# Kernel optimization log

Measured on AMD Instinct MI355X. Metric: run time of the kernel, lower is better.

## Reference

```python
import jax, jax.numpy as jnp
import numpy as np

B, T, E, H, V, K = 32, 256, 256, 256, 32000, 48
PAD = 0


def setup_inputs() -> dict:
    key = jax.random.key(0)
    ks = jax.random.split(key, 24)
    lengths = jnp.sort(jax.random.randint(ks[0], (B,), 1, T + 1))[::-1]
    lengths = lengths.at[0].set(T)  # pack_padded needs max length present
    sent = jax.random.randint(ks[1], (B, T), 1, V)
    pos = jnp.arange(T)[None, :]
    sentence = jnp.where(pos < lengths[:, None], sent, PAD)
    tags = jax.random.randint(ks[2], (B, T), 0, K)
    s = 0.1
    p = {"sentence": sentence, "lengths": lengths, "tags": tags}
    p["embed"] = jax.random.normal(ks[3], (V, E)) * s
    dims = [E, 2 * H]
    i = 4
    for l in range(2):
        for d in ("f", "b"):
            p[f"Wih_{l}{d}"] = jax.random.normal(ks[i], (4 * H, dims[l])) * s; i += 1
            p[f"Whh_{l}{d}"] = jax.random.normal(ks[i], (4 * H, H)) * s; i += 1
            p[f"b_{l}{d}"] = jax.random.normal(ks[i], (4 * H,)) * s; i += 1
    p["Wout"] = jax.random.normal(ks[i], (K, 2 * H)) * s; i += 1
    p["bout"] = jax.random.normal(ks[i], (K,)) * s; i += 1
    p["start_t"] = jax.random.normal(ks[i], (K,)) * s; i += 1
    p["end_t"] = jax.random.normal(ks[i], (K,)) * s; i += 1
    p["trans"] = jax.random.normal(ks[i], (K, K)) * s
    return p


def _lstm_dir(x, m, Wih, Whh, b, reverse):
    # x: [T,B,D] time-major, m: [T,B] bool. Masked update emulates pack_padded_sequence.
    if reverse:
        x, m = x[::-1], m[::-1]
    Bn, Hn = x.shape[1], Whh.shape[1]

    def step(carry, inp):
        h, c = carry
        xt, mt = inp
        g = xt @ Wih.T + h @ Whh.T + b
        i_, f_, g_, o_ = jnp.split(g, 4, axis=-1)
        c2 = jax.nn.sigmoid(f_) * c + jax.nn.sigmoid(i_) * jnp.tanh(g_)
        h2 = jax.nn.sigmoid(o_) * jnp.tanh(c2)
        mm = mt[:, None]
        h2 = jnp.where(mm, h2, h)
        c2 = jnp.where(mm, c2, c)
        return (h2, c2), jnp.where(mm, h2, 0.0)

    init = (jnp.zeros((Bn, Hn), x.dtype), jnp.zeros((Bn, Hn), x.dtype))
    _, hs = jax.lax.scan(step, init, (x, m))
    return hs[::-1] if reverse else hs


def _forward(sentence, tags, embed, layer_params, Wout, bout, start_t, end_t, trans):
    mask = sentence != PAD                      # [B,T]
    x = embed[sentence]                          # [B,T,E]
    xt = jnp.transpose(x, (1, 0, 2))             # [T,B,E]
    mt = mask.T                                  # [T,B]
    for (Wf, Uf, bf, Wb, Ub, bb) in layer_params:
        hf = _lstm_dir(xt, mt, Wf, Uf, bf, False)
        hb = _lstm_dir(xt, mt, Wb, Ub, bb, True)
        xt = jnp.concatenate([hf, hb], axis=-1)  # [T,B,2H]
    emit = xt @ Wout.T + bout                    # [T,B,K]; dropout is identity in eval

    # ---- CRF log-likelihood (torchcrf) ----
    mf = mt.astype(emit.dtype)
    tt = tags.T                                  # [T,B]
    bar = jnp.arange(sentence.shape[0])
    num = start_t[tt[0]] + emit[0, bar, tt[0]]

    def num_step(s, inp):
        em, tg, pg, m = inp
        return s + (trans[pg, tg] + em[bar, tg]) * m, None

    num, _ = jax.lax.scan(num_step, num, (emit[1:], tt[1:], tt[:-1], mf[1:]))
    last_idx = mf.sum(0).astype(jnp.int32) - 1
    last_tags = tt[last_idx, bar]
    num = num + end_t[last_tags]

    score = start_t[None, :] + emit[0]           # [B,K]

    def den_step(s, inp):
        em, m = inp
        nxt = jax.nn.logsumexp(s[:, :, None] + trans[None] + em[:, None, :], axis=1)
        return jnp.where(m[:, None] > 0, nxt, s), None

    score, _ = jax.lax.scan(den_step, score, (emit[1:], mf[1:]))
    den = jax.nn.logsumexp(score + end_t[None, :], axis=1)
    loss = (num - den).mean()                    # torchcrf reduction='mean' log-likelihood
    return jnp.transpose(emit, (1, 0, 2)), loss, mask


def reference(sentence, lengths, tags, embed,
              Wih_0f, Whh_0f, b_0f, Wih_0b, Whh_0b, b_0b,
              Wih_1f, Whh_1f, b_1f, Wih_1b, Whh_1b, b_1b,
              Wout, bout, start_t, end_t, trans):
    layers = [(Wih_0f, Whh_0f, b_0f, Wih_0b, Whh_0b, b_0b),
              (Wih_1f, Whh_1f, b_1f, Wih_1b, Whh_1b, b_1b)]
    return _forward(sentence, tags, embed, layers, Wout, bout, start_t, end_t, trans)
```

## Files before the change

kernel.cpp:

```cpp
#include <hip/hip_runtime.h>

#define Bz 32
#define Tz 256
#define Ez 256
#define Hz 256
#define Kz 48
#define G4 1024
#define H2 512

typedef __attribute__((ext_vector_type(8))) short short8;
typedef __attribute__((ext_vector_type(4))) float f32x4;
typedef unsigned short ushort_t;
typedef unsigned int uint_t;
typedef unsigned long long ull_t;

__device__ __forceinline__ float bf2f(ushort_t u) {
    unsigned int x = ((unsigned int)u) << 16;
    union { unsigned int i; float f; } c; c.i = x; return c.f;
}
__device__ __forceinline__ ushort_t f2bf(float f) {
    union { float f; unsigned int i; } c; c.f = f;
    unsigned int x = c.i;
    unsigned int lsb = (x >> 16) & 1u;
    x += 0x7fffu + lsb;
    return (ushort_t)(x >> 16);
}
__device__ __forceinline__ float sigm(float x) { return 1.f / (1.f + __expf(-x)); }
__device__ __forceinline__ float tanh_f(float x) { return 1.f - 2.f / (__expf(2.f * x) + 1.f); }

#define MFMA16(a, b, c) __builtin_amdgcn_mfma_f32_16x16x32_bf16((a), (b), (c), 0, 0, 0)

__device__ __forceinline__ void poll8_sweep(const ull_t* b0, const ull_t* b1,
                                            const ull_t* b2, const ull_t* b3,
                                            ull_t* o)
{
    asm volatile(
        "global_load_dwordx2 %0, %8, off sc0 sc1\n\t"
        "global_load_dwordx2 %1, %8, off offset:2048 sc0 sc1\n\t"
        "global_load_dwordx2 %2, %9, off sc0 sc1\n\t"
        "global_load_dwordx2 %3, %9, off offset:2048 sc0 sc1\n\t"
        "global_load_dwordx2 %4, %10, off sc0 sc1\n\t"
        "global_load_dwordx2 %5, %10, off offset:2048 sc0 sc1\n\t"
        "global_load_dwordx2 %6, %11, off sc0 sc1\n\t"
        "global_load_dwordx2 %7, %11, off offset:2048 sc0 sc1\n\t"
        "s_waitcnt vmcnt(0)"
        : "=&v"(o[0]), "=&v"(o[1]), "=&v"(o[2]), "=&v"(o[3]),
          "=&v"(o[4]), "=&v"(o[5]), "=&v"(o[6]), "=&v"(o[7])
        : "v"(b0), "v"(b1), "v"(b2), "v"(b3)
        : "memory");
}

struct CvtArgs {
    const float* s[9];
    ushort_t* d[9];
    int n[9];
};
__global__ __launch_bounds__(256) void cvt_all(CvtArgs a)
{
    int y = blockIdx.y;
    const float* src = a.s[y];
    ushort_t* dst = a.d[y];
    int n = a.n[y];
    int i = (blockIdx.x * 256 + threadIdx.x) * 4;
    if (i < n) {
        float4 v = *(const float4*)(src + i);
        ushort_t o[4] = { f2bf(v.x), f2bf(v.y), f2bf(v.z), f2bf(v.w) };
        *(uint2*)(dst + i) = *(uint2*)o;
    }
}

__global__ __launch_bounds__(64) void embed_kernel(
    const int* __restrict__ sent, const float* __restrict__ embed,
    ushort_t* __restrict__ emb, float* __restrict__ mask_out)
{
    int blk = blockIdx.x;
    int b = blk >> 8, t = blk & 255;
    int s = sent[blk];
    int tid = threadIdx.x;
    float4 v = *(const float4*)(embed + (size_t)s * Ez + tid * 4);
    ushort_t o[4] = { f2bf(v.x), f2bf(v.y), f2bf(v.z), f2bf(v.w) };
    *(uint2*)(emb + ((size_t)t * Bz + b) * Ez + tid * 4) = *(uint2*)o;
    if (tid == 0) mask_out[blk] = (s != 0) ? 1.0f : 0.0f;
}

__global__ __launch_bounds__(256) void gemm_xproj(
    const ushort_t* __restrict__ A,
    const ushort_t* __restrict__ Wf, const ushort_t* __restrict__ Wb,
    const float* __restrict__ biasf, const float* __restrict__ biasb,
    ushort_t* __restrict__ Cf, ushort_t* __restrict__ Cb,
    int M, int Kd)
{
    const ushort_t* W = blockIdx.z ? Wb : Wf;
    const float* bias = blockIdx.z ? biasb : biasf;
    ushort_t* C = blockIdx.z ? Cb : Cf;
    __shared__ __attribute__((aligned(16))) ushort_t sA[128 * 32];
    __shared__ __attribute__((aligned(16))) ushort_t sB[128 * 32];

    int m0 = blockIdx.x * 128, n0 = blockIdx.y * 128;
    int tid = threadIdx.x, l = tid & 63, w = tid >> 6;
    int lr = l & 15, lq = l >> 4;
    int mw = (w & 1) * 64, nw = (w >> 1) * 64;

    int srow_lane = l >> 2;
    int scol_lane = (l & 3) * 8;

    f32x4 acc[4][4] = {};
    for (int ko = 0; ko < Kd; ko += 32) {
        #pragma unroll
        for (int j = 0; j < 4; j++) {
            int seg = w * 4 + j;
            const ushort_t* src;
            ushort_t* dst;
            if (seg < 8) {
                src = A + (size_t)(m0 + seg * 16 + srow_lane) * Kd + ko + scol_lane;
                dst = sA + seg * 512;
            } else {
                src = W + (size_t)(n0 + (seg - 8) * 16 + srow_lane) * Kd + ko + scol_lane;
                dst = sB + (seg - 8) * 512;
            }
            __builtin_amdgcn_global_load_lds(src, dst, 16, 0, 0);
        }
        asm volatile("s_waitcnt vmcnt(0)" ::: "memory");
        __syncthreads();

        short8 af[4], bf_[4];
        #pragma unroll
        for (int mt = 0; mt < 4; mt++)
            af[mt] = *(const short8*)(&sA[(mw + mt * 16 + lr) * 32 + lq * 8]);
        #pragma unroll
        for (int nt = 0; nt < 4; nt++)
            bf_[nt] = *(const short8*)(&sB[(nw + nt * 16 + lr) * 32 + lq * 8]);
        #pragma unroll
        for (int mt = 0; mt < 4; mt++)
            #pragma unroll
            for (int nt = 0; nt < 4; nt++)
                acc[mt][nt] = MFMA16(af[mt], bf_[nt], acc[mt][nt]);
        __syncthreads();
    }

    #pragma unroll
    for (int mt = 0; mt < 4; mt++)
        #pragma unroll
        for (int nt = 0; nt < 4; nt++)
            #pragma unroll
            for (int r = 0; r < 4; r++) {
                int row = m0 + mw + mt * 16 + lq * 4 + r;
                int col = n0 + nw + nt * 16 + lr;
                float v = acc[mt][nt][r] + bias[col];
                C[(size_t)row * G4 + col] = f2bf(v);
            }
}

#define LDK 264

__global__ __launch_bounds__(256, 1) void lstm_layer(
    const ushort_t* __restrict__ Whh_f, const ushort_t* __restrict__ Whh_b,
    const ushort_t* __restrict__ Xp_f, const ushort_t* __restrict__ Xp_b,
    const int* __restrict__ lengths,
    ushort_t* __restrict__ hcat,
    ull_t* __restrict__ hbuf)
{
    __shared__ __attribute__((aligned(16))) ushort_t sH[Bz][LDK];
    __shared__ float sG[4][16][34];

    int bid = blockIdx.x;
    int dir = bid >> 4;
    int sub = bid & 15;
    int h0 = sub * 16;
    const ushort_t* Whh = dir ? Whh_b : Whh_f;
    const ushort_t* Xp  = dir ? Xp_b  : Xp_f;
    int tid = threadIdx.x, l = tid & 63, w = tid >> 6;
    int lr = l & 15, lq = l >> 4;
    int mw = (w & 1) * 16;
    int P  = w >> 1;
    int U0w = h0 + P * 8;

    short8 bw0[8], bw1[8];
    int gA = (lr & 3) * Hz + U0w + (lr >> 2);
    int gB = gA + 4;
    {
        const ushort_t* W0 = Whh + (size_t)gA * Hz;
        const ushort_t* W1 = Whh + (size_t)gB * Hz;
        #pragma unroll
        for (int k = 0; k < 8; k++) {
            bw0[k] = *(const short8*)(W0 + k * 32 + lq * 8);
            bw1[k] = *(const short8*)(W1 + k * 32 + lq * 8);
        }
    }

    int upd = (l < 32);
    int bloc = l & 15;
    int q = (l >> 4) & 1;
    int batch = mw + bloc;
    int lenb = lengths[batch];
    float c4[4] = {0.f, 0.f, 0.f, 0.f};
    ull_t prevw = 0;
    int pubw = batch * 64 + sub * 4 + P * 2 + q;
    int hcoff = dir * Hz + U0w + q * 4;

    for (int s = 0; s < Tz; s++) {
        int t_act = dir ? (Tz - 1 - s) : s;
        const ushort_t* Xrow = Xp + (size_t)t_act * Bz * G4;

        float xv0[4], xv1[4];
        #pragma unroll
        for (int r = 0; r < 4; r++) {
            int brow = mw + lq * 4 + r;
            xv0[r] = bf2f(Xrow[(size_t)brow * G4 + gA]);
            xv1[r] = bf2f(Xrow[(size_t)brow * G4 + gB]);
        }

        const ull_t* hcur = hbuf + ((s & 1) * 2 + dir) * (Bz * Hz / 4);
        const ull_t* b0 = hcur + tid;
        const ull_t* b1 = b0 + 512;
        const ull_t* b2 = b0 + 1024;
        const ull_t* b3 = b0 + 1536;
        uint_t tagc = (uint_t)(((s >> 1) ^ s) & 1);
        ull_t vals[8];
        for (;;) {
            poll8_sweep(b0, b1, b2, b3, vals);
            uint_t ok = 1u;
            #pragma unroll
            for (int k = 0; k < 8; k++)
                ok &= (((uint_t)(vals[k] >> 14) & 1u) == tagc);
            if (ok) break;
        }
        #pragma unroll
        for (int k = 0; k < 8; k++) {
            int idx = k * 256 + tid;
            *(ull_t*)(&sH[idx >> 6][(idx & 63) * 4]) = vals[k] & ~(1ull << 14);
        }
        __syncthreads();

        f32x4 acc0 = {}, acc1 = {};
        #pragma unroll
        for (int k = 0; k < 8; k++) {
            short8 a = *(const short8*)(&sH[mw + lr][k * 32 + lq * 8]);
            acc0 = MFMA16(a, bw0[k], acc0);
            acc1 = MFMA16(a, bw1[k], acc1);
        }
        #pragma unroll
        for (int r = 0; r < 4; r++) {
            sG[w][lq * 4 + r][lr]      = acc0[r] + xv0[r];
            sG[w][lq * 4 + r][16 + lr] = acc1[r] + xv1[r];
        }
        asm volatile("s_waitcnt lgkmcnt(0)" ::: "memory");

        uint_t tagp = (uint_t)((((s + 1) >> 1) ^ (s + 1)) & 1);
        if (upd) {
            int msk = (t_act < lenb);
            ushort_t hx[4], hc[4];
            const ushort_t* ho = (const ushort_t*)&prevw;
            #pragma unroll
            for (int j = 0; j < 4; j++) {
                int cb = q * 16 + j * 4;
                float gi = sG[w][bloc][cb], gf = sG[w][bloc][cb + 1];
                float gg = sG[w][bloc][cb + 2], go = sG[w][bloc][cb + 3];
                float c2 = sigm(gf) * c4[j] + sigm(gi) * tanh_f(gg);
                float h2 = sigm(go) * tanh_f(c2);
                if (msk) c4[j] = c2;
                ushort_t hn = f2bf(h2);
                hx[j] = msk ? hn : ho[j];
                hc[j] = msk ? hn : (ushort_t)0;
            }
            ull_t wd; __builtin_memcpy(&wd, hx, 8);
            prevw = wd;
            wd |= ((ull_t)tagp) << 14;
            ull_t* hnxt = hbuf + (((s + 1) & 1) * 2 + dir) * (Bz * Hz / 4);
            __hip_atomic_store(&hnxt[pubw], wd,
                               __ATOMIC_RELAXED, __HIP_MEMORY_SCOPE_AGENT);
            ull_t wc; __builtin_memcpy(&wc, hc, 8);
            *(ull_t*)(hcat + ((size_t)t_act * Bz + batch) * H2 + hcoff) = wc;
        }
    }
}

__global__ __launch_bounds__(256) void gemm_emit(
    const ushort_t* __restrict__ A, const ushort_t* __restrict__ Wout,
    const float* __restrict__ bout, float* __restrict__ emit_out)
{
    int tid = threadIdx.x, l = tid & 63, w = tid >> 6;
    int m0 = blockIdx.x * 64 + w * 16;
    int lr = l & 15, lq = l >> 4;
    f32x4 acc[3] = {};
    for (int ko = 0; ko < H2; ko += 32) {
        short8 a = *(const short8*)(A + (size_t)(m0 + lr) * H2 + ko + lq * 8);
        #pragma unroll
        for (int nt = 0; nt < 3; nt++) {
            short8 bfr = *(const short8*)(Wout + (size_t)(nt * 16 + lr) * H2 + ko + lq * 8);
            acc[nt] = MFMA16(a, bfr, acc[nt]);
        }
    }
    #pragma unroll
    for (int nt = 0; nt < 3; nt++)
        #pragma unroll
        for (int r = 0; r < 4; r++) {
            int row = m0 + lq * 4 + r;
            int col = nt * 16 + lr;
            float v = acc[nt][r] + bout[col];
            int t = row >> 5, b = row & 31;
            emit_out[((size_t)b * Tz + t) * Kz + col] = v;
        }
}

__global__ __launch_bounds__(256) void crf_num(
    const float* __restrict__ emit, const int* __restrict__ sent,
    const int* __restrict__ tags, const int* __restrict__ lengths,
    const float* __restrict__ trans, const float* __restrict__ start_t,
    const float* __restrict__ end_t, float* __restrict__ num)
{
    __shared__ float red[4];
    int b = blockIdx.x, t = threadIdx.x;
    int tg = tags[b * Tz + t];
    float term;
    if (t == 0) {
        term = start_t[tg] + emit[(size_t)b * Tz * Kz + tg];
        int len = lengths[b];
        term += end_t[tags[b * Tz + len - 1]];
    } else if (sent[b * Tz + t] != 0) {
        int tp = tags[b * Tz + t - 1];
        term = trans[tp * Kz + tg] + emit[((size_t)b * Tz + t) * Kz + tg];
    } else term = 0.f;
    #pragma unroll
    for (int off = 1; off < 64; off <<= 1) term += __shfl_xor(term, off);
    int w = t >> 6;
    if ((t & 63) == 0) red[w] = term;
    __syncthreads();
    if (t == 0) num[b] = red[0] + red[1] + red[2] + red[3];
}

__global__ __launch_bounds__(64) void crf_den(
    const float* __restrict__ emit, const int* __restrict__ lengths,
    const float* __restrict__ trans, const float* __restrict__ start_t,
    const float* __restrict__ end_t, float* __restrict__ den)
{
    __shared__ float sT[Kz * Kz];
    __shared__ float sS[Kz];
    int b = blockIdx.x, l = threadIdx.x;
    for (int i = l; i < Kz * Kz; i += 64) sT[i] = trans[i];
    int len = lengths[b];
    bool act = l < Kz;
    float s = act ? (start_t[l] + emit[(size_t)b * Tz * Kz + l]) : -1e30f;
    for (int t = 1; t < len; t++) {
        float em = act ? emit[((size_t)b * Tz + t) * Kz + l] : 0.f;
        if (act) sS[l] = s;
        float M = s;
        #pragma unroll
        for (int off = 1; off < 64; off <<= 1) M = fmaxf(M, __shfl_xor(M, off));
        float a0 = 0.f, a1 = 0.f, a2 = 0.f, a3 = 0.f;
        #pragma unroll 4
        for (int i = 0; i < Kz; i += 4) {
            a0 += __expf(sS[i]     + sT[i * Kz + l]       - M);
            a1 += __expf(sS[i + 1] + sT[(i + 1) * Kz + l] - M);
            a2 += __expf(sS[i + 2] + sT[(i + 2) * Kz + l] - M);
            a3 += __expf(sS[i + 3] + sT[(i + 3) * Kz + l] - M);
        }
        float sum = (a0 + a1) + (a2 + a3);
        if (act) s = em + M + __logf(sum);
    }
    float v = act ? (s + end_t[l]) : -1e30f;
    float M = v;
    #pragma unroll
    for (int off = 1; off < 64; off <<= 1) M = fmaxf(M, __shfl_xor(M, off));
    float accv = act ? __expf(v - M) : 0.f;
    #pragma unroll
    for (int off = 1; off < 64; off <<= 1) accv += __shfl_xor(accv, off);
    if (l == 0) den[b] = M + __logf(accv);
}

__global__ __launch_bounds__(64) void crf_loss(
    const float* __restrict__ num, const float* __restrict__ den, float* __restrict__ out)
{
    int l = threadIdx.x;
    float v = (l < Bz) ? (num[l] - den[l]) : 0.f;
    #pragma unroll
    for (int off = 1; off < 64; off <<= 1) v += __shfl_xor(v, off);
    if (l == 0) out[0] = v / (float)Bz;
}

extern "C" void kernel_launch(void* const* d_in, const int* in_sizes, int n_in,
                              void* d_out, int out_size, void* d_ws, size_t ws_size,
                              hipStream_t stream) {
    const int* sent      = (const int*)d_in[0];
    const int* lengths   = (const int*)d_in[1];
    const int* tags      = (const int*)d_in[2];
    const float* embed   = (const float*)d_in[3];
    const float* Wih0f = (const float*)d_in[4];
    const float* Whh0f = (const float*)d_in[5];
    const float* b0f   = (const float*)d_in[6];
    const float* Wih0b = (const float*)d_in[7];
    const float* Whh0b = (const float*)d_in[8];
    const float* b0b   = (const float*)d_in[9];
    const float* Wih1f = (const float*)d_in[10];
    const float* Whh1f = (const float*)d_in[11];
    const float* b1f   = (const float*)d_in[12];
    const float* Wih1b = (const float*)d_in[13];
    const float* Whh1b = (const float*)d_in[14];
    const float* b1b   = (const float*)d_in[15];
    const float* Wout  = (const float*)d_in[16];
    const float* bout  = (const float*)d_in[17];
    const float* start_t = (const float*)d_in[18];
    const float* end_t   = (const float*)d_in[19];
    const float* trans   = (const float*)d_in[20];

    char* ws = (char*)d_ws;
    ushort_t* Xp_f  = (ushort_t*)(ws);
    ushort_t* Xp_b  = (ushort_t*)(ws + 16777216);
    ushort_t* hcat  = (ushort_t*)(ws + 33554432);
    ushort_t* emb   = (ushort_t*)(ws + 41943040);
    ushort_t* Whh0f_c = (ushort_t*)(ws + 46137344);
    ushort_t* Whh0b_c = (ushort_t*)(ws + 46661632);
    ushort_t* Wih0f_c = (ushort_t*)(ws + 47185920);
    ushort_t* Wih0b_c = (ushort_t*)(ws + 47710208);
    ushort_t* Wih1f_c = (ushort_t*)(ws + 48234496);
    ushort_t* Wih1b_c = (ushort_t*)(ws + 49283072);
    ushort_t* Whh1f_c = (ushort_t*)(ws + 50331648);
    ushort_t* Whh1b_c = (ushort_t*)(ws + 50855936);
    ushort_t* Wout_c  = (ushort_t*)(ws + 51380224);
    ull_t*    hbufL0 = (ull_t*)(ws + 51429376);
    ull_t*    hbufL1 = (ull_t*)(ws + 51560448);
    float*    num   = (float*)   (ws + 51691520);
    float*    den   = (float*)   (ws + 51691776);

    float* out      = (float*)d_out;
    float* loss_out = out + (size_t)Bz * Tz * Kz;
    float* mask_out = loss_out + 1;

    hipMemsetAsync(hbufL0, 0, 262144, stream);

    CvtArgs ca;
    ca.s[0] = Whh0f; ca.d[0] = Whh0f_c; ca.n[0] = 262144;
    ca.s[1] = Whh0b; ca.d[1] = Whh0b_c; ca.n[1] = 262144;
    ca.s[2] = Wih0f; ca.d[2] = Wih0f_c; ca.n[2] = 262144;
    ca.s[3] = Wih0b; ca.d[3] = Wih0b_c; ca.n[3] = 262144;
    ca.s[4] = Wih1f; ca.d[4] = Wih1f_c; ca.n[4] = 524288;
    ca.s[5] = Wih1b; ca.d[5] = Wih1b_c; ca.n[5] = 524288;
    ca.s[6] = Whh1f; ca.d[6] = Whh1f_c; ca.n[6] = 262144;
    ca.s[7] = Whh1b; ca.d[7] = Whh1b_c; ca.n[7] = 262144;
    ca.s[8] = Wout;  ca.d[8] = Wout_c;  ca.n[8] = 24576;
    cvt_all<<<dim3(512, 9), 256, 0, stream>>>(ca);

    embed_kernel<<<Bz * Tz, 64, 0, stream>>>(sent, embed, emb, mask_out);

    gemm_xproj<<<dim3(Tz * Bz / 128, G4 / 128, 2), 256, 0, stream>>>(
        emb, Wih0f_c, Wih0b_c, b0f, b0b, Xp_f, Xp_b, Tz * Bz, Ez);

    lstm_layer<<<32, 256, 0, stream>>>(Whh0f_c, Whh0b_c, Xp_f, Xp_b, lengths, hcat, hbufL0);

    gemm_xproj<<<dim3(Tz * Bz / 128, G4 / 128, 2), 256, 0, stream>>>(
        hcat, Wih1f_c, Wih1b_c, b1f, b1b, Xp_f, Xp_b, Tz * Bz, H2);

    lstm_layer<<<32, 256, 0, stream>>>(Whh1f_c, Whh1b_c, Xp_f, Xp_b, lengths, hcat, hbufL1);

    gemm_emit<<<Tz * Bz / 64, 256, 0, stream>>>(hcat, Wout_c, bout, out);

    crf_num<<<Bz, 256, 0, stream>>>(out, sent, tags, lengths, trans, start_t, end_t, num);
    crf_den<<<Bz, 64, 0, stream>>>(out, lengths, trans, start_t, end_t, den);
    crf_loss<<<1, 64, 0, stream>>>(num, den, loss_out);
}
```

Baseline: 1.661 ms.

## Fuse CRF numerator and denominator kernels, split logsumexp over four waves

Merges the CRF numerator and denominator kernels into one 256-thread launch. The forward-algorithm recurrence now spreads the 48-term reduction per tag across four wavefronts of 12 terms each, combined through shared memory. This removes one launch and shortens the serial per-step exp chain, but adds two block-wide barriers per time step. The CRF part is small next to the LSTM layers, so the effect on total time is likely minor.

```diff
diff --git a/kernel.cpp b/kernel.cpp
--- a/kernel.cpp
+++ b/kernel.cpp
@@ -303,19 +303,27 @@
         }
 }
 
-__global__ __launch_bounds__(256) void crf_num(
+__global__ __launch_bounds__(256) void crf_numden(
     const float* __restrict__ emit, const int* __restrict__ sent,
     const int* __restrict__ tags, const int* __restrict__ lengths,
     const float* __restrict__ trans, const float* __restrict__ start_t,
-    const float* __restrict__ end_t, float* __restrict__ num)
+    const float* __restrict__ end_t, float* __restrict__ num,
+    float* __restrict__ den)
 {
     __shared__ float red[4];
+    __shared__ float sT[Kz * Kz];
+    __shared__ float sS[Kz];
+    __shared__ float sP[4][Kz];
     int b = blockIdx.x, t = threadIdx.x;
+    int w = t >> 6, l = t & 63;
+    int len = lengths[b];
+
+    for (int i = t; i < Kz * Kz; i += 256) sT[i] = trans[i];
+
     int tg = tags[b * Tz + t];
     float term;
     if (t == 0) {
         term = start_t[tg] + emit[(size_t)b * Tz * Kz + tg];
-        int len = lengths[b];
         term += end_t[tags[b * Tz + len - 1]];
     } else if (sent[b * Tz + t] != 0) {
         int tp = tags[b * Tz + t - 1];
@@ -323,49 +331,42 @@
     } else term = 0.f;
     #pragma unroll
     for (int off = 1; off < 64; off <<= 1) term += __shfl_xor(term, off);
-    int w = t >> 6;
-    if ((t & 63) == 0) red[w] = term;
+    if (l == 0) red[w] = term;
+
+    bool act = l < Kz;
+    if (w == 0 && act) sS[l] = start_t[l] + emit[(size_t)b * Tz * Kz + l];
     __syncthreads();
     if (t == 0) num[b] = red[0] + red[1] + red[2] + red[3];
-}
-
-__global__ __launch_bounds__(64) void crf_den(
-    const float* __restrict__ emit, const int* __restrict__ lengths,
-    const float* __restrict__ trans, const float* __restrict__ start_t,
-    const float* __restrict__ end_t, float* __restrict__ den)
-{
-    __shared__ float sT[Kz * Kz];
-    __shared__ float sS[Kz];
-    int b = blockIdx.x, l = threadIdx.x;
-    for (int i = l; i < Kz * Kz; i += 64) sT[i] = trans[i];
-    int len = lengths[b];
-    bool act = l < Kz;
-    float s = act ? (start_t[l] + emit[(size_t)b * Tz * Kz + l]) : -1e30f;
-    for (int t = 1; t < len; t++) {
-        float em = act ? emit[((size_t)b * Tz + t) * Kz + l] : 0.f;
-        if (act) sS[l] = s;
-        float M = s;
+
+    int i0 = w * 12;
+    for (int tt = 1; tt < len; tt++) {
+        float sv = act ? sS[l] : -1e30f;
+        float M = sv;
         #pragma unroll
         for (int off = 1; off < 64; off <<= 1) M = fmaxf(M, __shfl_xor(M, off));
-        float a0 = 0.f, a1 = 0.f, a2 = 0.f, a3 = 0.f;
-        #pragma unroll 4
-        for (int i = 0; i < Kz; i += 4) {
-            a0 += __expf(sS[i]     + sT[i * Kz + l]       - M);
-            a1 += __expf(sS[i + 1] + sT[(i + 1) * Kz + l] - M);
-            a2 += __expf(sS[i + 2] + sT[(i + 2) * Kz + l] - M);
-            a3 += __expf(sS[i + 3] + sT[(i + 3) * Kz + l] - M);
-        }
-        float sum = (a0 + a1) + (a2 + a3);
-        if (act) s = em + M + __logf(sum);
-    }
-    float v = act ? (s + end_t[l]) : -1e30f;
-    float M = v;
-    #pragma unroll
-    for (int off = 1; off < 64; off <<= 1) M = fmaxf(M, __shfl_xor(M, off));
-    float accv = act ? __expf(v - M) : 0.f;
-    #pragma unroll
-    for (int off = 1; off < 64; off <<= 1) accv += __shfl_xor(accv, off);
-    if (l == 0) den[b] = M + __logf(accv);
+        float a = 0.f;
+        #pragma unroll
+        for (int i = 0; i < 12; i++)
+            a += __expf(sS[i0 + i] + sT[(i0 + i) * Kz + l] - M);
+        if (act) sP[w][l] = a;
+        __syncthreads();
+        if (w == 0 && act) {
+            float sum = (sP[0][l] + sP[1][l]) + (sP[2][l] + sP[3][l]);
+            float em = emit[((size_t)b * Tz + tt) * Kz + l];
+            sS[l] = em + M + __logf(sum);
+        }
+        __syncthreads();
+    }
+    if (w == 0) {
+        float v = act ? (sS[l] + end_t[l]) : -1e30f;
+        float M = v;
+        #pragma unroll
+        for (int off = 1; off < 64; off <<= 1) M = fmaxf(M, __shfl_xor(M, off));
+        float accv = act ? __expf(v - M) : 0.f;
+        #pragma unroll
+        for (int off = 1; off < 64; off <<= 1) accv += __shfl_xor(accv, off);
+        if (l == 0) den[b] = M + __logf(accv);
+    }
 }
 
 __global__ __launch_bounds__(64) void crf_loss(
@@ -454,7 +455,6 @@
 
     gemm_emit<<<Tz * Bz / 64, 256, 0, stream>>>(hcat, Wout_c, bout, out);
 
-    crf_num<<<Bz, 256, 0, stream>>>(out, sent, tags, lengths, trans, start_t, end_t, num);
-    crf_den<<<Bz, 64, 0, stream>>>(out, lengths, trans, start_t, end_t, den);
+    crf_numden<<<Bz, 256, 0, stream>>>(out, sent, tags, lengths, trans, start_t, end_t, num, den);
     crf_loss<<<1, 64, 0, stream>>>(num, den, loss_out);
 }
```

Result: faster. 1.627 ms (-2.1%).
